# Kernel optimization log

Hardware: AMD Instinct MI355X
Metric: run time of the kernel (lower is better)

Reference implementation:

```python
import jax, jax.numpy as jnp
import numpy as np

LN_EPS = 1e-5

def _lstm_scan(xp, w_hh):
    # xp: [T, B, 4H] precomputed input projections (+bias); w_hh: [4H, H]
    H = w_hh.shape[1]
    B = xp.shape[1]
    def step(carry, x_t):
        h, c = carry
        gates = x_t + h @ w_hh.T
        i, f, g, o = jnp.split(gates, 4, axis=-1)  # torch gate order i,f,g,o
        i = jax.nn.sigmoid(i); f = jax.nn.sigmoid(f)
        g = jnp.tanh(g); o = jax.nn.sigmoid(o)
        c = f * c + i * g
        h = o * jnp.tanh(c)
        return (h, c), h
    init = (jnp.zeros((B, H), xp.dtype), jnp.zeros((B, H), xp.dtype))
    _, hs = jax.lax.scan(step, init, xp)
    return hs  # [T, B, H]

def setup_inputs() -> dict:
    key = jax.random.key(0)
    ks = jax.random.split(key, 16)
    B, T, V, E, K = 64, 512, 21128, 256, 9
    H4 = 4 * E
    s = 0.08  # small init scale for numerical stability
    return {
        'word_ids': jax.random.randint(ks[0], (B, T), 0, V, dtype=jnp.int32),
        'label_ids': jax.random.randint(ks[1], (B, T), 0, K, dtype=jnp.int32),
        'embed_table': jax.random.normal(ks[2], (V, E), jnp.float32) * s,
        'w_ih_f': jax.random.normal(ks[3], (H4, E), jnp.float32) * s,
        'w_hh_f': jax.random.normal(ks[4], (H4, E), jnp.float32) * s,
        'b_f': jnp.zeros((H4,), jnp.float32),
        'w_ih_b': jax.random.normal(ks[5], (H4, E), jnp.float32) * s,
        'w_hh_b': jax.random.normal(ks[6], (H4, E), jnp.float32) * s,
        'b_b': jnp.zeros((H4,), jnp.float32),
        'ln_gamma': jnp.ones((2 * E,), jnp.float32),
        'ln_beta': jnp.zeros((2 * E,), jnp.float32),
        'cls_w': jax.random.normal(ks[7], (K, 2 * E), jnp.float32) * s,
        'cls_b': jnp.zeros((K,), jnp.float32),
        'crf_start': jax.random.normal(ks[8], (K,), jnp.float32) * 0.1,
        'crf_end': jax.random.normal(ks[9], (K,), jnp.float32) * 0.1,
        'crf_trans': jax.random.normal(ks[10], (K, K), jnp.float32) * 0.1,
    }

def reference(word_ids, label_ids, embed_table, w_ih_f, w_hh_f, b_f,
              w_ih_b, w_hh_b, b_b, ln_gamma, ln_beta, cls_w, cls_b,
              crf_start, crf_end, crf_trans):
    # Embedding (dropout is identity at eval)
    emb = embed_table[word_ids]                      # [B, T, E]

    # BiLSTM: precompute input projections once, scan over time
    xf = (emb @ w_ih_f.T + b_f).transpose(1, 0, 2)   # [T, B, 4H]
    hf = _lstm_scan(xf, w_hh_f)                      # [T, B, H]
    xb = (emb[:, ::-1] @ w_ih_b.T + b_b).transpose(1, 0, 2)
    hb = _lstm_scan(xb, w_hh_b)[::-1]                # reverse back to forward time
    seq = jnp.concatenate([hf, hb], axis=-1).transpose(1, 0, 2)  # [B, T, 2H]

    # LayerNorm over last dim
    mu = seq.mean(-1, keepdims=True)
    var = ((seq - mu) ** 2).mean(-1, keepdims=True)
    seq = (seq - mu) * jax.lax.rsqrt(var + LN_EPS) * ln_gamma + ln_beta

    logits = seq @ cls_w.T + cls_b                   # [B, T, K] = CRF emissions

    # --- CRF log-likelihood (no mask: all positions valid) ---
    tags = label_ids
    # numerator: score of gold path
    em_score = jnp.take_along_axis(logits, tags[..., None], axis=-1)[..., 0]  # [B, T]
    trans_score = crf_trans[tags[:, :-1], tags[:, 1:]].sum(axis=1)            # [B]
    numerator = (crf_start[tags[:, 0]] + em_score.sum(axis=1)
                 + trans_score + crf_end[tags[:, -1]])                        # [B]

    # denominator: forward algorithm (logsumexp DP over time)
    alpha0 = crf_start[None, :] + logits[:, 0]       # [B, K]
    em_rest = logits[:, 1:].transpose(1, 0, 2)       # [T-1, B, K]
    def step(alpha, em_t):
        # alpha: [B, K] (prev tag), crf_trans: [K, K], em_t: [B, K] (next tag)
        new = jax.scipy.special.logsumexp(
            alpha[:, :, None] + crf_trans[None, :, :] + em_t[:, None, :], axis=1)
        return new, None
    alpha, _ = jax.lax.scan(step, alpha0, em_rest)
    logZ = jax.scipy.special.logsumexp(alpha + crf_end[None, :], axis=1)      # [B]

    llh = (numerator - logZ).sum()   # torchcrf default reduction='sum'
    loss = -llh
    preds = jnp.argmax(logits, axis=-1)
    return (loss, preds)
```

## Files before the change

kernel.cpp:

```cpp
#include <hip/hip_runtime.h>
#include <cstdint>
#include <cmath>

typedef __attribute__((ext_vector_type(8))) short short8;
typedef __attribute__((ext_vector_type(4))) float floatx4;

__device__ __forceinline__ unsigned pk_bf16(float x, float y) {
    unsigned ux = __float_as_uint(x); ux = ux + 0x7fffu + ((ux >> 16) & 1u);
    unsigned uy = __float_as_uint(y); uy = uy + 0x7fffu + ((uy >> 16) & 1u);
    return (ux >> 16) | (uy & 0xffff0000u);
}
__device__ __forceinline__ unsigned short bf16r(float x) {
    unsigned ux = __float_as_uint(x);
    return (unsigned short)((ux + 0x7fffu + ((ux >> 16) & 1u)) >> 16);
}
__device__ __forceinline__ float bf16d(unsigned short v) {
    return __uint_as_float((unsigned)v << 16);
}

__device__ __forceinline__ float fsigmoid(float x) {
    return __builtin_amdgcn_rcpf(1.f + __expf(-x));
}
__device__ __forceinline__ float ftanh(float x) {
    return 1.f - 2.f * __builtin_amdgcn_rcpf(__expf(2.f * x) + 1.f);
}

__device__ __forceinline__ void bar_lds() {
    __builtin_amdgcn_sched_barrier(0);
    asm volatile("s_waitcnt lgkmcnt(0)" ::: "memory");
    __builtin_amdgcn_s_barrier();
    __builtin_amdgcn_sched_barrier(0);
}

__global__ __launch_bounds__(256) void proj_kernel(
    const int* __restrict__ word_ids, const float* __restrict__ embed,
    const float* __restrict__ w_ih_f, const float* __restrict__ b_f,
    const float* __restrict__ w_ih_b, const float* __restrict__ b_b,
    unsigned short* __restrict__ XF, unsigned short* __restrict__ XB,
    int t0, int lgL)
{
    __shared__ unsigned short As[64][264];
    __shared__ unsigned short Bs[64][264];
    __shared__ int idx[64];

    const int tid = threadIdx.x;
    const int nt  = blockIdx.x;
    const int dir = blockIdx.y;
    const int Lm1 = (1 << lgL) - 1;
    const float* __restrict__ W    = dir ? w_ih_b : w_ih_f;
    const float* __restrict__ bias = dir ? b_b : b_f;
    unsigned short* __restrict__ Xout = dir ? XB : XF;

    if (tid < 64) {
        int n  = nt * 64 + tid;
        int b  = n >> lgL;
        int tl = n & Lm1;
        int tg = dir ? (511 - (t0 + tl)) : (t0 + tl);
        idx[tid] = word_ids[b * 512 + tg];
    }
    __syncthreads();

    #pragma unroll
    for (int i = 0; i < 16; ++i) {
        int flat = i * 256 + tid;
        int r  = flat >> 6;
        int kq = flat & 63;
        floatx4 a = *(const floatx4*)&embed[(size_t)idx[r] * 256 + kq * 4];
        *(uint2*)&As[r][kq * 4] = make_uint2(pk_bf16(a.x, a.y), pk_bf16(a.z, a.w));
    }
    __syncthreads();

    const int w    = tid >> 6;
    const int lane = tid & 63;
    const int q    = lane >> 4;
    const int lr   = lane & 15;

    short8 af[8];
    #pragma unroll
    for (int ks = 0; ks < 8; ++ks)
        af[ks] = *(const short8*)&As[w * 16 + lr][ks * 32 + q * 8];

    int bb[4], tt4[4];
    #pragma unroll
    for (int reg = 0; reg < 4; ++reg) {
        int n  = nt * 64 + w * 16 + q * 4 + reg;
        bb[reg]  = n >> lgL;
        tt4[reg] = n & Lm1;
    }

    for (int jt = 0; jt < 16; ++jt) {
        __syncthreads();
        #pragma unroll
        for (int i = 0; i < 16; ++i) {
            int flat = i * 256 + tid;
            int r  = flat >> 6;
            int kq = flat & 63;
            floatx4 wv = *(const floatx4*)&W[(size_t)(jt * 64 + r) * 256 + kq * 4];
            *(uint2*)&Bs[r][kq * 4] = make_uint2(pk_bf16(wv.x, wv.y), pk_bf16(wv.z, wv.w));
        }
        __syncthreads();

        #pragma unroll
        for (int jt4 = 0; jt4 < 4; ++jt4) {
            floatx4 c = {0.f, 0.f, 0.f, 0.f};
            #pragma unroll
            for (int ks = 0; ks < 8; ++ks) {
                short8 bf = *(const short8*)&Bs[jt4 * 16 + lr][ks * 32 + q * 8];
                c = __builtin_amdgcn_mfma_f32_16x16x32_bf16(af[ks], bf, c, 0, 0, 0);
            }
            int j = jt * 64 + jt4 * 16 + lr;
            float bj = bias[j];
            #pragma unroll
            for (int reg = 0; reg < 4; ++reg)
                Xout[((size_t)tt4[reg] * 64 + bb[reg]) * 1024 + j] = bf16r(c[reg] + bj);
        }
    }
}

#define LSTM_STEP(T, P, XG)                                                   \
    {                                                                         \
        floatx4 c[4][2];                                                      \
        _Pragma("unroll")                                                     \
        for (int gt = 0; gt < 4; ++gt) { c[gt][0] = zero; c[gt][1] = zero; }  \
        _Pragma("unroll")                                                     \
        for (int ks = 0; ks < 8; ++ks) {                                      \
            short8 af = *(const short8*)&Ah[P][lr & 1][ks * 32 + q * 8];      \
            _Pragma("unroll")                                                 \
            for (int nt = 0; nt < 8; ++nt) {                                  \
                const int gt = nt >> 1, ut = nt & 1;                          \
                short8 bf = (nt < 6) ? wreg[nt][ks]                           \
                                     : Wlds[((w * 2 + (nt - 6)) * 8 + ks) * 64 + lane]; \
                c[gt][ut] = __builtin_amdgcn_mfma_f32_16x16x32_bf16(          \
                    af, bf, c[gt][ut], 0, 0, 0);                              \
            }                                                                 \
        }                                                                     \
        float gsum[4];                                                        \
        _Pragma("unroll")                                                     \
        for (int gt = 0; gt < 4; ++gt) {                                      \
            float a0 = bsel ? c[gt][0][1] : c[gt][0][0];                      \
            float a1 = bsel ? c[gt][1][1] : c[gt][1][0];                      \
            gsum[gt] = (utsel ? a1 : a0) + XG[gt];                            \
        }                                                                     \
        {   \
            int tn = ((T) + 2 < t1) ? ((T) + 2 - t0) : 0;                     \
            const unsigned short* Xc =                                        \
                &X[((size_t)tn * 64 + B0 + b_own) * 1024 + u_own];            \
            _Pragma("unroll")                                                 \
            for (int gg = 0; gg < 4; ++gg) XG[gg] = bf16d(Xc[gg * 256]);      \
        }                                                                     \
        {                                                                     \
            float ig = fsigmoid(gsum[0]);                                     \
            float fg = fsigmoid(gsum[1]);                                     \
            float gc = ftanh(gsum[2]);                                        \
            float og = fsigmoid(gsum[3]);                                     \
            cst = fg * cst + ig * gc;                                         \
            float h = og * ftanh(cst);                                        \
            hlast = h;                                                        \
            Ah[(P) ^ 1][b_own][u_own] = bf16r(h);                             \
            int tt = dir ? (511 - (T)) : (T);                                 \
            Hout[((size_t)tt * 64 + B0 + b_own) * 256 + u_own] = h;           \
        }                                                                     \
        bar_lds();                                                            \
    }

__global__ __launch_bounds__(512, 1)
__attribute__((amdgpu_num_vgpr(256)))
void lstm_scan(
    const unsigned short* __restrict__ XF, const unsigned short* __restrict__ XB,
    const float* __restrict__ w_hh_f, const float* __restrict__ w_hh_b,
    float* __restrict__ hf, float* __restrict__ hb,
    float* __restrict__ state_c, float* __restrict__ state_h, int t0, int t1)
{
    __shared__ unsigned short Ah[2][2][264];
    __shared__ short8 Wlds[8 * 2 * 8 * 64];

    const int blk = blockIdx.x;
    const int dir = blk >> 5;
    const int grp = blk & 31;
    const int B0  = grp * 2;
    const unsigned short* __restrict__ X = dir ? XB : XF;
    const float* __restrict__ Whh = dir ? w_hh_b : w_hh_f;
    float* __restrict__ Hout      = dir ? hb : hf;

    const int tid  = threadIdx.x;
    const int w    = tid >> 6;
    const int lane = tid & 63;
    const int q    = lane >> 4;
    const int lr   = lane & 15;

    short8 wreg[6][8];
    #pragma unroll
    for (int nt = 0; nt < 8; ++nt) {
        const int gt = nt >> 1, ut = nt & 1;
        const float* wrow = &Whh[(size_t)(gt * 256 + w * 32 + ut * 16 + lr) * 256];
        #pragma unroll
        for (int ks = 0; ks < 8; ++ks) {
            floatx4 a = *(const floatx4*)&wrow[ks * 32 + q * 8];
            floatx4 b = *(const floatx4*)&wrow[ks * 32 + q * 8 + 4];
            union { uint4 u4; short8 s; } cv;
            cv.u4 = make_uint4(pk_bf16(a.x, a.y), pk_bf16(a.z, a.w),
                               pk_bf16(b.x, b.y), pk_bf16(b.z, b.w));
            if (nt < 6) wreg[nt][ks] = cv.s;
            else        Wlds[((w * 2 + (nt - 6)) * 8 + ks) * 64 + lane] = cv.s;
        }
    }

    const int b_own = lane >> 5;
    const int u_own = w * 32 + (lane & 31);
    const int sgi   = (dir * 64 + B0 + b_own) * 256 + u_own;

    float cst = 0.f, hlast = 0.f;
    if (t0 != 0) { cst = state_c[sgi]; hlast = state_h[sgi]; }
    Ah[t0 & 1][b_own][u_own] = bf16r(hlast);

    float xga[4], xgb[4];
    {
        const unsigned short* Xc0 = &X[((size_t)(B0 + b_own)) * 1024 + u_own];
        #pragma unroll
        for (int gg = 0; gg < 4; ++gg) xga[gg] = bf16d(Xc0[gg * 256]);
        const unsigned short* Xc1 = &X[((size_t)(64 + B0 + b_own)) * 1024 + u_own];
        #pragma unroll
        for (int gg = 0; gg < 4; ++gg) xgb[gg] = bf16d(Xc1[gg * 256]);
    }
    bar_lds();

    const floatx4 zero = {0.f, 0.f, 0.f, 0.f};
    const bool utsel = ((lane >> 4) & 1) != 0;
    const bool bsel  = (lane >> 5) != 0;

    for (int t = t0; t < t1; t += 2) {
        LSTM_STEP(t,     0, xga)
        LSTM_STEP(t + 1, 1, xgb)
    }

    state_c[sgi] = cst;
    state_h[sgi] = hlast;
}

__global__ __launch_bounds__(256) void ln_cls_kernel(
    const float* __restrict__ hf, const float* __restrict__ hb,
    const float* __restrict__ gamma, const float* __restrict__ beta,
    const float* __restrict__ cls_w, const float* __restrict__ cls_b,
    float* __restrict__ logits, float* __restrict__ dout)
{
    const int lane = threadIdx.x & 63;
    const int wid  = threadIdx.x >> 6;
    const int pos  = blockIdx.x * 4 + wid;
    const int b = pos >> 9;
    const int t = pos & 511;

    float4 v0 = *(const float4*)&hf[((size_t)t * 64 + b) * 256 + lane * 4];
    float4 v1 = *(const float4*)&hb[((size_t)t * 64 + b) * 256 + lane * 4];
    float x[8] = {v0.x, v0.y, v0.z, v0.w, v1.x, v1.y, v1.z, v1.w};

    float s = 0.f;
    #pragma unroll
    for (int i = 0; i < 8; ++i) s += x[i];
    #pragma unroll
    for (int off = 32; off > 0; off >>= 1) s += __shfl_xor(s, off, 64);
    float mu = s * (1.f / 512.f);

    float d[8];
    float sq = 0.f;
    #pragma unroll
    for (int i = 0; i < 8; ++i) { d[i] = x[i] - mu; sq += d[i] * d[i]; }
    #pragma unroll
    for (int off = 32; off > 0; off >>= 1) sq += __shfl_xor(sq, off, 64);
    float rs = 1.f / sqrtf(sq * (1.f / 512.f) + 1e-5f);

    float4 g0  = *(const float4*)&gamma[lane * 4];
    float4 g1  = *(const float4*)&gamma[256 + lane * 4];
    float4 be0 = *(const float4*)&beta[lane * 4];
    float4 be1 = *(const float4*)&beta[256 + lane * 4];
    float y[8];
    y[0] = d[0] * rs * g0.x + be0.x; y[1] = d[1] * rs * g0.y + be0.y;
    y[2] = d[2] * rs * g0.z + be0.z; y[3] = d[3] * rs * g0.w + be0.w;
    y[4] = d[4] * rs * g1.x + be1.x; y[5] = d[5] * rs * g1.y + be1.y;
    y[6] = d[6] * rs * g1.z + be1.z; y[7] = d[7] * rs * g1.w + be1.w;

    float lgt[9];
    #pragma unroll
    for (int c = 0; c < 9; ++c) {
        float4 w0 = *(const float4*)&cls_w[c * 512 + lane * 4];
        float4 w1 = *(const float4*)&cls_w[c * 512 + 256 + lane * 4];
        float p = y[0] * w0.x + y[1] * w0.y + y[2] * w0.z + y[3] * w0.w
                + y[4] * w1.x + y[5] * w1.y + y[6] * w1.z + y[7] * w1.w;
        #pragma unroll
        for (int off = 32; off > 0; off >>= 1) p += __shfl_xor(p, off, 64);
        lgt[c] = p + cls_b[c];
    }
    if (lane == 0) {
        int bestc = 0;
        float bestv = lgt[0];
        #pragma unroll
        for (int c = 1; c < 9; ++c)
            if (lgt[c] > bestv) { bestv = lgt[c]; bestc = c; }
        dout[1 + pos] = (float)bestc;
        #pragma unroll
        for (int c = 0; c < 9; ++c) logits[(size_t)pos * 9 + c] = lgt[c];
    }
}

__global__ __launch_bounds__(64) void crf_kernel(
    const float* __restrict__ logits, const int* __restrict__ label_ids,
    const float* __restrict__ crf_start, const float* __restrict__ crf_end,
    const float* __restrict__ crf_trans, float* __restrict__ llh)
{
    __shared__ float Ts[9][12];
    const int b = blockIdx.x;
    const int lane = threadIdx.x;
    if (lane < 81) Ts[lane / 9][lane % 9] = crf_trans[lane];
    __syncthreads();

    const float* __restrict__ em  = &logits[(size_t)b * 512 * 9];
    const int* __restrict__ tags  = &label_ids[b * 512];

    float part = 0.f;
    for (int t = lane; t < 512; t += 64) {
        int tg = tags[t];
        part += em[t * 9 + tg];
        if (t < 511) part += Ts[tg][tags[t + 1]];
    }
    #pragma unroll
    for (int off = 32; off > 0; off >>= 1) part += __shfl_xor(part, off, 64);
    float numer = part + crf_start[tags[0]] + crf_end[tags[511]];

    const int j = (lane < 9) ? lane : 0;
    float alpha = crf_start[j] + em[j];
    for (int t = 1; t < 512; ++t) {
        float av[9];
        float m = -1e30f;
        #pragma unroll
        for (int i = 0; i < 9; ++i) {
            float ai = __shfl(alpha, i, 64);
            av[i] = ai + Ts[i][j];
            m = fmaxf(m, av[i]);
        }
        float ssum = 0.f;
        #pragma unroll
        for (int i = 0; i < 9; ++i) ssum += expf(av[i] - m);
        alpha = m + logf(ssum) + em[t * 9 + j];
    }
    float v = (lane < 9) ? (alpha + crf_end[j]) : -1e30f;
    float mm = v;
    #pragma unroll
    for (int off = 32; off > 0; off >>= 1) mm = fmaxf(mm, __shfl_xor(mm, off, 64));
    float es = (lane < 9) ? expf(v - mm) : 0.f;
    #pragma unroll
    for (int off = 32; off > 0; off >>= 1) es += __shfl_xor(es, off, 64);
    if (lane == 0) llh[b] = numer - (mm + logf(es));
}

__global__ __launch_bounds__(64) void final_reduce(
    const float* __restrict__ llh, float* __restrict__ dout)
{
    float v = llh[threadIdx.x];
    #pragma unroll
    for (int off = 32; off > 0; off >>= 1) v += __shfl_xor(v, off, 64);
    if (threadIdx.x == 0) dout[0] = -v;
}

extern "C" void kernel_launch(void* const* d_in, const int* in_sizes, int n_in,
                              void* d_out, int out_size, void* d_ws, size_t ws_size,
                              hipStream_t stream)
{
    const int*   word_ids  = (const int*)d_in[0];
    const int*   label_ids = (const int*)d_in[1];
    const float* embed     = (const float*)d_in[2];
    const float* w_ih_f    = (const float*)d_in[3];
    const float* w_hh_f    = (const float*)d_in[4];
    const float* b_f       = (const float*)d_in[5];
    const float* w_ih_b    = (const float*)d_in[6];
    const float* w_hh_b    = (const float*)d_in[7];
    const float* b_b       = (const float*)d_in[8];
    const float* ln_gamma  = (const float*)d_in[9];
    const float* ln_beta   = (const float*)d_in[10];
    const float* cls_w     = (const float*)d_in[11];
    const float* cls_b     = (const float*)d_in[12];
    const float* crf_start = (const float*)d_in[13];
    const float* crf_end   = (const float*)d_in[14];
    const float* crf_trans = (const float*)d_in[15];

    char* w = (char*)d_ws;
    auto alloc = [&](size_t bytes) -> char* {
        char* p = w; w += (bytes + 255) & ~(size_t)255; return p;
    };
    float* hf      = (float*)alloc((size_t)8388608 * 4);
    float* hb      = (float*)alloc((size_t)8388608 * 4);
    float* logits  = (float*)alloc((size_t)294912 * 4);
    float* state_c = (float*)alloc((size_t)32768 * 4);
    float* state_h = (float*)alloc((size_t)32768 * 4);
    float* llh     = (float*)alloc((size_t)64 * 4);
    size_t fixed   = (size_t)(w - (char*)d_ws);

    int L = 512;
    while (L > 32 && fixed + (size_t)L * 262144 > ws_size) L >>= 1;
    unsigned short* XF = (unsigned short*)alloc((size_t)L * 65536 * 2);
    unsigned short* XB = (unsigned short*)alloc((size_t)L * 65536 * 2);
    int lgL = 31 - __builtin_clz((unsigned)L);

    for (int t0 = 0; t0 < 512; t0 += L) {
        proj_kernel<<<dim3(L, 2), 256, 0, stream>>>(
            word_ids, embed, w_ih_f, b_f, w_ih_b, b_b, XF, XB, t0, lgL);
        lstm_scan<<<64, 512, 0, stream>>>(
            XF, XB, w_hh_f, w_hh_b, hf, hb, state_c, state_h, t0, t0 + L);
    }
    ln_cls_kernel<<<8192, 256, 0, stream>>>(
        hf, hb, ln_gamma, ln_beta, cls_w, cls_b, logits, (float*)d_out);
    crf_kernel<<<64, 64, 0, stream>>>(
        logits, label_ids, crf_start, crf_end, crf_trans, llh);
    final_reduce<<<1, 64, 0, stream>>>(llh, (float*)d_out);
}
```

Measured before the change: 1.394 ms.

## Overlap next-chunk input projection with LSTM scan in one fused launch

The time axis is split into four fixed chunks of 128 steps, with double-buffered projection outputs. Each launch runs the recurrent scan for chunk c in 64 blocks while extra blocks compute the bf16 input projections for chunk c+1, so projection work hides behind the latency-bound serial scan instead of running between scans. It also fixes the chunk size regardless of workspace and raises shared memory per block to about 133 KB to fit two GEMM units. The risk is that projection blocks compete with scan blocks for memory bandwidth and CU resources, and the chunked scan adds launch and state save/restore overhead.

```diff
diff --git a/kernel.cpp b/kernel.cpp
--- a/kernel.cpp
+++ b/kernel.cpp
@@ -165,76 +165,166 @@
 
 __global__ __launch_bounds__(512, 1)
 __attribute__((amdgpu_num_vgpr(256)))
-void lstm_scan(
-    const unsigned short* __restrict__ XF, const unsigned short* __restrict__ XB,
+void fused_scan_proj(
+    const unsigned short* __restrict__ XFc, const unsigned short* __restrict__ XBc,
     const float* __restrict__ w_hh_f, const float* __restrict__ w_hh_b,
     float* __restrict__ hf, float* __restrict__ hb,
-    float* __restrict__ state_c, float* __restrict__ state_h, int t0, int t1)
+    float* __restrict__ state_c, float* __restrict__ state_h, int t0, int t1,
+    const int* __restrict__ word_ids, const float* __restrict__ embed,
+    const float* __restrict__ w_ih_f, const float* __restrict__ b_f,
+    const float* __restrict__ w_ih_b, const float* __restrict__ b_b,
+    unsigned short* __restrict__ XFn, unsigned short* __restrict__ XBn,
+    int pt0, int lgL)
 {
-    __shared__ unsigned short Ah[2][2][264];
-    __shared__ short8 Wlds[8 * 2 * 8 * 64];
-
-    const int blk = blockIdx.x;
-    const int dir = blk >> 5;
-    const int grp = blk & 31;
-    const int B0  = grp * 2;
-    const unsigned short* __restrict__ X = dir ? XB : XF;
-    const float* __restrict__ Whh = dir ? w_hh_b : w_hh_f;
-    float* __restrict__ Hout      = dir ? hb : hf;
-
-    const int tid  = threadIdx.x;
-    const int w    = tid >> 6;
-    const int lane = tid & 63;
-    const int q    = lane >> 4;
-    const int lr   = lane & 15;
-
-    short8 wreg[6][8];
-    #pragma unroll
-    for (int nt = 0; nt < 8; ++nt) {
-        const int gt = nt >> 1, ut = nt & 1;
-        const float* wrow = &Whh[(size_t)(gt * 256 + w * 32 + ut * 16 + lr) * 256];
-        #pragma unroll
-        for (int ks = 0; ks < 8; ++ks) {
-            floatx4 a = *(const floatx4*)&wrow[ks * 32 + q * 8];
-            floatx4 b = *(const floatx4*)&wrow[ks * 32 + q * 8 + 4];
-            union { uint4 u4; short8 s; } cv;
-            cv.u4 = make_uint4(pk_bf16(a.x, a.y), pk_bf16(a.z, a.w),
-                               pk_bf16(b.x, b.y), pk_bf16(b.z, b.w));
-            if (nt < 6) wreg[nt][ks] = cv.s;
-            else        Wlds[((w * 2 + (nt - 6)) * 8 + ks) * 64 + lane] = cv.s;
-        }
-    }
-
-    const int b_own = lane >> 5;
-    const int u_own = w * 32 + (lane & 31);
-    const int sgi   = (dir * 64 + B0 + b_own) * 256 + u_own;
-
-    float cst = 0.f, hlast = 0.f;
-    if (t0 != 0) { cst = state_c[sgi]; hlast = state_h[sgi]; }
-    Ah[t0 & 1][b_own][u_own] = bf16r(hlast);
-
-    float xga[4], xgb[4];
-    {
-        const unsigned short* Xc0 = &X[((size_t)(B0 + b_own)) * 1024 + u_own];
-        #pragma unroll
-        for (int gg = 0; gg < 4; ++gg) xga[gg] = bf16d(Xc0[gg * 256]);
-        const unsigned short* Xc1 = &X[((size_t)(64 + B0 + b_own)) * 1024 + u_own];
-        #pragma unroll
-        for (int gg = 0; gg < 4; ++gg) xgb[gg] = bf16d(Xc1[gg * 256]);
-    }
-    bar_lds();
-
-    const floatx4 zero = {0.f, 0.f, 0.f, 0.f};
-    const bool utsel = ((lane >> 4) & 1) != 0;
-    const bool bsel  = (lane >> 5) != 0;
-
-    for (int t = t0; t < t1; t += 2) {
-        LSTM_STEP(t,     0, xga)
-        LSTM_STEP(t + 1, 1, xgb)
-    }
-
-    state_c[sgi] = cst;
-    state_h[sgi] = hlast;
+    __shared__ __align__(16) char smem[135936];
+
+    if (blockIdx.x < 64) {
+        unsigned short (*Ah)[2][264] = (unsigned short (*)[2][264])smem;
+        short8* Wlds = (short8*)(smem + 2112);
+
+        const int blk = blockIdx.x;
+        const int dir = blk >> 5;
+        const int grp = blk & 31;
+        const int B0  = grp * 2;
+        const unsigned short* __restrict__ X = dir ? XBc : XFc;
+        const float* __restrict__ Whh = dir ? w_hh_b : w_hh_f;
+        float* __restrict__ Hout      = dir ? hb : hf;
+
+        const int tid  = threadIdx.x;
+        const int w    = tid >> 6;
+        const int lane = tid & 63;
+        const int q    = lane >> 4;
+        const int lr   = lane & 15;
+
+        short8 wreg[6][8];
+        #pragma unroll
+        for (int nt = 0; nt < 8; ++nt) {
+            const int gt = nt >> 1, ut = nt & 1;
+            const float* wrow = &Whh[(size_t)(gt * 256 + w * 32 + ut * 16 + lr) * 256];
+            #pragma unroll
+            for (int ks = 0; ks < 8; ++ks) {
+                floatx4 a = *(const floatx4*)&wrow[ks * 32 + q * 8];
+                floatx4 b = *(const floatx4*)&wrow[ks * 32 + q * 8 + 4];
+                union { uint4 u4; short8 s; } cv;
+                cv.u4 = make_uint4(pk_bf16(a.x, a.y), pk_bf16(a.z, a.w),
+                                   pk_bf16(b.x, b.y), pk_bf16(b.z, b.w));
+                if (nt < 6) wreg[nt][ks] = cv.s;
+                else        Wlds[((w * 2 + (nt - 6)) * 8 + ks) * 64 + lane] = cv.s;
+            }
+        }
+
+        const int b_own = lane >> 5;
+        const int u_own = w * 32 + (lane & 31);
+        const int sgi   = (dir * 64 + B0 + b_own) * 256 + u_own;
+
+        float cst = 0.f, hlast = 0.f;
+        if (t0 != 0) { cst = state_c[sgi]; hlast = state_h[sgi]; }
+        Ah[t0 & 1][b_own][u_own] = bf16r(hlast);
+
+        float xga[4], xgb[4];
+        {
+            const unsigned short* Xc0 = &X[((size_t)(B0 + b_own)) * 1024 + u_own];
+            #pragma unroll
+            for (int gg = 0; gg < 4; ++gg) xga[gg] = bf16d(Xc0[gg * 256]);
+            const unsigned short* Xc1 = &X[((size_t)(64 + B0 + b_own)) * 1024 + u_own];
+            #pragma unroll
+            for (int gg = 0; gg < 4; ++gg) xgb[gg] = bf16d(Xc1[gg * 256]);
+        }
+        bar_lds();
+
+        const floatx4 zero = {0.f, 0.f, 0.f, 0.f};
+        const bool utsel = ((lane >> 4) & 1) != 0;
+        const bool bsel  = (lane >> 5) != 0;
+
+        for (int t = t0; t < t1; t += 2) {
+            LSTM_STEP(t,     0, xga)
+            LSTM_STEP(t + 1, 1, xgb)
+        }
+
+        state_c[sgi] = cst;
+        state_h[sgi] = hlast;
+    } else {
+        const int unit = threadIdx.x >> 8;
+        const int tid  = threadIdx.x & 255;
+        const int uidx = (blockIdx.x - 64) * 2 + unit;
+        const int dir  = uidx & 1;
+        const int nt   = uidx >> 1;
+        const int Lm1  = (1 << lgL) - 1;
+
+        char* base = smem + unit * 67968;
+        unsigned short (*As)[264] = (unsigned short (*)[264])base;
+        unsigned short (*Bs)[264] = (unsigned short (*)[264])(base + 33792);
+        int* idx = (int*)(base + 67584);
+
+        const float* __restrict__ W    = dir ? w_ih_b : w_ih_f;
+        const float* __restrict__ bias = dir ? b_b : b_f;
+        unsigned short* __restrict__ Xout = dir ? XBn : XFn;
+
+        if (tid < 64) {
+            int n  = nt * 64 + tid;
+            int b  = n >> lgL;
+            int tl = n & Lm1;
+            int tg = dir ? (511 - (pt0 + tl)) : (pt0 + tl);
+            idx[tid] = word_ids[b * 512 + tg];
+        }
+        __syncthreads();
+
+        #pragma unroll
+        for (int i = 0; i < 16; ++i) {
+            int flat = i * 256 + tid;
+            int r  = flat >> 6;
+            int kq = flat & 63;
+            floatx4 a = *(const floatx4*)&embed[(size_t)idx[r] * 256 + kq * 4];
+            *(uint2*)&As[r][kq * 4] = make_uint2(pk_bf16(a.x, a.y), pk_bf16(a.z, a.w));
+        }
+        __syncthreads();
+
+        const int w    = tid >> 6;
+        const int lane = tid & 63;
+        const int q    = lane >> 4;
+        const int lr   = lane & 15;
+
+        short8 af[8];
+        #pragma unroll
+        for (int ks = 0; ks < 8; ++ks)
+            af[ks] = *(const short8*)&As[w * 16 + lr][ks * 32 + q * 8];
+
+        int bb[4], tt4[4];
+        #pragma unroll
+        for (int reg = 0; reg < 4; ++reg) {
+            int n  = nt * 64 + w * 16 + q * 4 + reg;
+            bb[reg]  = n >> lgL;
+            tt4[reg] = n & Lm1;
+        }
+
+        for (int jt = 0; jt < 16; ++jt) {
+            __syncthreads();
+            #pragma unroll
+            for (int i = 0; i < 16; ++i) {
+                int flat = i * 256 + tid;
+                int r  = flat >> 6;
+                int kq = flat & 63;
+                floatx4 wv = *(const floatx4*)&W[(size_t)(jt * 64 + r) * 256 + kq * 4];
+                *(uint2*)&Bs[r][kq * 4] = make_uint2(pk_bf16(wv.x, wv.y), pk_bf16(wv.z, wv.w));
+            }
+            __syncthreads();
+
+            #pragma unroll
+            for (int jt4 = 0; jt4 < 4; ++jt4) {
+                floatx4 c = {0.f, 0.f, 0.f, 0.f};
+                #pragma unroll
+                for (int ks = 0; ks < 8; ++ks) {
+                    short8 bf = *(const short8*)&Bs[jt4 * 16 + lr][ks * 32 + q * 8];
+                    c = __builtin_amdgcn_mfma_f32_16x16x32_bf16(af[ks], bf, c, 0, 0, 0);
+                }
+                int j = jt * 64 + jt4 * 16 + lr;
+                float bj = bias[j];
+                #pragma unroll
+                for (int reg = 0; reg < 4; ++reg)
+                    Xout[((size_t)tt4[reg] * 64 + bb[reg]) * 1024 + j] = bf16r(c[reg] + bj);
+            }
+        }
+    }
 }
 
 __global__ __launch_bounds__(256) void ln_cls_kernel(
@@ -391,20 +481,29 @@
     float* state_c = (float*)alloc((size_t)32768 * 4);
     float* state_h = (float*)alloc((size_t)32768 * 4);
     float* llh     = (float*)alloc((size_t)64 * 4);
-    size_t fixed   = (size_t)(w - (char*)d_ws);
-
-    int L = 512;
-    while (L > 32 && fixed + (size_t)L * 262144 > ws_size) L >>= 1;
-    unsigned short* XF = (unsigned short*)alloc((size_t)L * 65536 * 2);
-    unsigned short* XB = (unsigned short*)alloc((size_t)L * 65536 * 2);
-    int lgL = 31 - __builtin_clz((unsigned)L);
-
-    for (int t0 = 0; t0 < 512; t0 += L) {
-        proj_kernel<<<dim3(L, 2), 256, 0, stream>>>(
-            word_ids, embed, w_ih_f, b_f, w_ih_b, b_b, XF, XB, t0, lgL);
-        lstm_scan<<<64, 512, 0, stream>>>(
-            XF, XB, w_hh_f, w_hh_b, hf, hb, state_c, state_h, t0, t0 + L);
-    }
+
+    const int L   = 128;
+    const int lgL = 7;
+    const size_t chunkElems = (size_t)L * 65536;
+    unsigned short* XF = (unsigned short*)alloc(2 * chunkElems * 2);
+    unsigned short* XB = (unsigned short*)alloc(2 * chunkElems * 2);
+
+    proj_kernel<<<dim3(L, 2), 256, 0, stream>>>(
+        word_ids, embed, w_ih_f, b_f, w_ih_b, b_b, XF, XB, 0, lgL);
+
+    for (int c = 0; c < 4; ++c) {
+        const unsigned short* XFc = XF + (size_t)(c & 1) * chunkElems;
+        const unsigned short* XBc = XB + (size_t)(c & 1) * chunkElems;
+        unsigned short* XFn = XF + (size_t)((c + 1) & 1) * chunkElems;
+        unsigned short* XBn = XB + (size_t)((c + 1) & 1) * chunkElems;
+        int grid = (c < 3) ? 64 + L : 64;
+        fused_scan_proj<<<grid, 512, 0, stream>>>(
+            XFc, XBc, w_hh_f, w_hh_b, hf, hb, state_c, state_h,
+            c * L, (c + 1) * L,
+            word_ids, embed, w_ih_f, b_f, w_ih_b, b_b, XFn, XBn,
+            (c + 1) * L, lgL);
+    }
+
     ln_cls_kernel<<<8192, 256, 0, stream>>>(
         hf, hb, ln_gamma, ln_beta, cls_w, cls_b, logits, (float*)d_out);
     crf_kernel<<<64, 64, 0, stream>>>(
```

After: 1.580 ms. 1.13x slower.

## Fuse input projection and LSTM scan into one persistent producer-consumer kernel

Applied to the files above, without the earlier changes.

Merges the projection GEMM and the recurrent LSTM scan into a single persistent launch. 64 blocks run the scan while 128 blocks compute input projections in 128-step chunks and signal readiness through atomic flags. The scan waits on each chunk's flag, so projection of later chunks overlaps the serial recurrence and the separate launches plus carried-state round trips go away. The design relies on all 192 blocks being co-resident to avoid deadlock, needs full-length X buffers, and drops the chunked fallback for small workspaces.

```diff
diff --git a/kernel.cpp b/kernel.cpp
--- a/kernel.cpp
+++ b/kernel.cpp
@@ -30,91 +30,6 @@
     asm volatile("s_waitcnt lgkmcnt(0)" ::: "memory");
     __builtin_amdgcn_s_barrier();
     __builtin_amdgcn_sched_barrier(0);
-}
-
-__global__ __launch_bounds__(256) void proj_kernel(
-    const int* __restrict__ word_ids, const float* __restrict__ embed,
-    const float* __restrict__ w_ih_f, const float* __restrict__ b_f,
-    const float* __restrict__ w_ih_b, const float* __restrict__ b_b,
-    unsigned short* __restrict__ XF, unsigned short* __restrict__ XB,
-    int t0, int lgL)
-{
-    __shared__ unsigned short As[64][264];
-    __shared__ unsigned short Bs[64][264];
-    __shared__ int idx[64];
-
-    const int tid = threadIdx.x;
-    const int nt  = blockIdx.x;
-    const int dir = blockIdx.y;
-    const int Lm1 = (1 << lgL) - 1;
-    const float* __restrict__ W    = dir ? w_ih_b : w_ih_f;
-    const float* __restrict__ bias = dir ? b_b : b_f;
-    unsigned short* __restrict__ Xout = dir ? XB : XF;
-
-    if (tid < 64) {
-        int n  = nt * 64 + tid;
-        int b  = n >> lgL;
-        int tl = n & Lm1;
-        int tg = dir ? (511 - (t0 + tl)) : (t0 + tl);
-        idx[tid] = word_ids[b * 512 + tg];
-    }
-    __syncthreads();
-
-    #pragma unroll
-    for (int i = 0; i < 16; ++i) {
-        int flat = i * 256 + tid;
-        int r  = flat >> 6;
-        int kq = flat & 63;
-        floatx4 a = *(const floatx4*)&embed[(size_t)idx[r] * 256 + kq * 4];
-        *(uint2*)&As[r][kq * 4] = make_uint2(pk_bf16(a.x, a.y), pk_bf16(a.z, a.w));
-    }
-    __syncthreads();
-
-    const int w    = tid >> 6;
-    const int lane = tid & 63;
-    const int q    = lane >> 4;
-    const int lr   = lane & 15;
-
-    short8 af[8];
-    #pragma unroll
-    for (int ks = 0; ks < 8; ++ks)
-        af[ks] = *(const short8*)&As[w * 16 + lr][ks * 32 + q * 8];
-
-    int bb[4], tt4[4];
-    #pragma unroll
-    for (int reg = 0; reg < 4; ++reg) {
-        int n  = nt * 64 + w * 16 + q * 4 + reg;
-        bb[reg]  = n >> lgL;
-        tt4[reg] = n & Lm1;
-    }
-
-    for (int jt = 0; jt < 16; ++jt) {
-        __syncthreads();
-        #pragma unroll
-        for (int i = 0; i < 16; ++i) {
-            int flat = i * 256 + tid;
-            int r  = flat >> 6;
-            int kq = flat & 63;
-            floatx4 wv = *(const floatx4*)&W[(size_t)(jt * 64 + r) * 256 + kq * 4];
-            *(uint2*)&Bs[r][kq * 4] = make_uint2(pk_bf16(wv.x, wv.y), pk_bf16(wv.z, wv.w));
-        }
-        __syncthreads();
-
-        #pragma unroll
-        for (int jt4 = 0; jt4 < 4; ++jt4) {
-            floatx4 c = {0.f, 0.f, 0.f, 0.f};
-            #pragma unroll
-            for (int ks = 0; ks < 8; ++ks) {
-                short8 bf = *(const short8*)&Bs[jt4 * 16 + lr][ks * 32 + q * 8];
-                c = __builtin_amdgcn_mfma_f32_16x16x32_bf16(af[ks], bf, c, 0, 0, 0);
-            }
-            int j = jt * 64 + jt4 * 16 + lr;
-            float bj = bias[j];
-            #pragma unroll
-            for (int reg = 0; reg < 4; ++reg)
-                Xout[((size_t)tt4[reg] * 64 + bb[reg]) * 1024 + j] = bf16r(c[reg] + bj);
-        }
-    }
 }
 
 #define LSTM_STEP(T, P, XG)                                                   \
@@ -141,8 +56,8 @@
             float a1 = bsel ? c[gt][1][1] : c[gt][1][0];                      \
             gsum[gt] = (utsel ? a1 : a0) + XG[gt];                            \
         }                                                                     \
-        {   \
-            int tn = ((T) + 2 < t1) ? ((T) + 2 - t0) : 0;                     \
+        {               \
+            int tn = ((T) + 2 < 512) ? ((T) + 2) : 0;                         \
             const unsigned short* Xc =                                        \
                 &X[((size_t)tn * 64 + B0 + b_own) * 1024 + u_own];            \
             _Pragma("unroll")                                                 \
@@ -165,76 +80,183 @@
 
 __global__ __launch_bounds__(512, 1)
 __attribute__((amdgpu_num_vgpr(256)))
-void lstm_scan(
-    const unsigned short* __restrict__ XF, const unsigned short* __restrict__ XB,
+void fused_persistent(
+    unsigned short* __restrict__ XF, unsigned short* __restrict__ XB,
     const float* __restrict__ w_hh_f, const float* __restrict__ w_hh_b,
     float* __restrict__ hf, float* __restrict__ hb,
-    float* __restrict__ state_c, float* __restrict__ state_h, int t0, int t1)
+    const int* __restrict__ word_ids, const float* __restrict__ embed,
+    const float* __restrict__ w_ih_f, const float* __restrict__ b_f,
+    const float* __restrict__ w_ih_b, const float* __restrict__ b_b,
+    int* __restrict__ flags)
 {
-    __shared__ unsigned short Ah[2][2][264];
-    __shared__ short8 Wlds[8 * 2 * 8 * 64];
-
-    const int blk = blockIdx.x;
-    const int dir = blk >> 5;
-    const int grp = blk & 31;
-    const int B0  = grp * 2;
-    const unsigned short* __restrict__ X = dir ? XB : XF;
-    const float* __restrict__ Whh = dir ? w_hh_b : w_hh_f;
-    float* __restrict__ Hout      = dir ? hb : hf;
-
-    const int tid  = threadIdx.x;
-    const int w    = tid >> 6;
-    const int lane = tid & 63;
-    const int q    = lane >> 4;
-    const int lr   = lane & 15;
-
-    short8 wreg[6][8];
-    #pragma unroll
-    for (int nt = 0; nt < 8; ++nt) {
-        const int gt = nt >> 1, ut = nt & 1;
-        const float* wrow = &Whh[(size_t)(gt * 256 + w * 32 + ut * 16 + lr) * 256];
-        #pragma unroll
-        for (int ks = 0; ks < 8; ++ks) {
-            floatx4 a = *(const floatx4*)&wrow[ks * 32 + q * 8];
-            floatx4 b = *(const floatx4*)&wrow[ks * 32 + q * 8 + 4];
-            union { uint4 u4; short8 s; } cv;
-            cv.u4 = make_uint4(pk_bf16(a.x, a.y), pk_bf16(a.z, a.w),
-                               pk_bf16(b.x, b.y), pk_bf16(b.z, b.w));
-            if (nt < 6) wreg[nt][ks] = cv.s;
-            else        Wlds[((w * 2 + (nt - 6)) * 8 + ks) * 64 + lane] = cv.s;
-        }
-    }
-
-    const int b_own = lane >> 5;
-    const int u_own = w * 32 + (lane & 31);
-    const int sgi   = (dir * 64 + B0 + b_own) * 256 + u_own;
-
-    float cst = 0.f, hlast = 0.f;
-    if (t0 != 0) { cst = state_c[sgi]; hlast = state_h[sgi]; }
-    Ah[t0 & 1][b_own][u_own] = bf16r(hlast);
-
-    float xga[4], xgb[4];
-    {
-        const unsigned short* Xc0 = &X[((size_t)(B0 + b_own)) * 1024 + u_own];
-        #pragma unroll
-        for (int gg = 0; gg < 4; ++gg) xga[gg] = bf16d(Xc0[gg * 256]);
-        const unsigned short* Xc1 = &X[((size_t)(64 + B0 + b_own)) * 1024 + u_own];
-        #pragma unroll
-        for (int gg = 0; gg < 4; ++gg) xgb[gg] = bf16d(Xc1[gg * 256]);
-    }
-    bar_lds();
-
-    const floatx4 zero = {0.f, 0.f, 0.f, 0.f};
-    const bool utsel = ((lane >> 4) & 1) != 0;
-    const bool bsel  = (lane >> 5) != 0;
-
-    for (int t = t0; t < t1; t += 2) {
-        LSTM_STEP(t,     0, xga)
-        LSTM_STEP(t + 1, 1, xgb)
-    }
-
-    state_c[sgi] = cst;
-    state_h[sgi] = hlast;
+    __shared__ __align__(16) char smem[135936];
+
+    if (blockIdx.x < 64) {
+        unsigned short (*Ah)[2][264] = (unsigned short (*)[2][264])smem;
+        short8* Wlds = (short8*)(smem + 2112);
+
+        const int blk = blockIdx.x;
+        const int dir = blk >> 5;
+        const int grp = blk & 31;
+        const int B0  = grp * 2;
+        const unsigned short* __restrict__ X = dir ? XB : XF;
+        const float* __restrict__ Whh = dir ? w_hh_b : w_hh_f;
+        float* __restrict__ Hout      = dir ? hb : hf;
+
+        const int tid  = threadIdx.x;
+        const int w    = tid >> 6;
+        const int lane = tid & 63;
+        const int q    = lane >> 4;
+        const int lr   = lane & 15;
+
+        short8 wreg[6][8];
+        #pragma unroll
+        for (int nt = 0; nt < 8; ++nt) {
+            const int gt = nt >> 1, ut = nt & 1;
+            const float* wrow = &Whh[(size_t)(gt * 256 + w * 32 + ut * 16 + lr) * 256];
+            #pragma unroll
+            for (int ks = 0; ks < 8; ++ks) {
+                floatx4 a = *(const floatx4*)&wrow[ks * 32 + q * 8];
+                floatx4 b = *(const floatx4*)&wrow[ks * 32 + q * 8 + 4];
+                union { uint4 u4; short8 s; } cv;
+                cv.u4 = make_uint4(pk_bf16(a.x, a.y), pk_bf16(a.z, a.w),
+                                   pk_bf16(b.x, b.y), pk_bf16(b.z, b.w));
+                if (nt < 6) wreg[nt][ks] = cv.s;
+                else        Wlds[((w * 2 + (nt - 6)) * 8 + ks) * 64 + lane] = cv.s;
+            }
+        }
+
+        if (tid == 0) {
+            while (__hip_atomic_load(&flags[0], __ATOMIC_ACQUIRE,
+                                     __HIP_MEMORY_SCOPE_AGENT) < 128)
+                __builtin_amdgcn_s_sleep(2);
+        }
+        __syncthreads();
+
+        const int b_own = lane >> 5;
+        const int u_own = w * 32 + (lane & 31);
+
+        float cst = 0.f, hlast = 0.f;
+        Ah[0][b_own][u_own] = 0;
+
+        float xga[4], xgb[4];
+        {
+            const unsigned short* Xc0 = &X[((size_t)(B0 + b_own)) * 1024 + u_own];
+            #pragma unroll
+            for (int gg = 0; gg < 4; ++gg) xga[gg] = bf16d(Xc0[gg * 256]);
+            const unsigned short* Xc1 = &X[((size_t)(64 + B0 + b_own)) * 1024 + u_own];
+            #pragma unroll
+            for (int gg = 0; gg < 4; ++gg) xgb[gg] = bf16d(Xc1[gg * 256]);
+        }
+        bar_lds();
+
+        const floatx4 zero = {0.f, 0.f, 0.f, 0.f};
+        const bool utsel = ((lane >> 4) & 1) != 0;
+        const bool bsel  = (lane >> 5) != 0;
+
+        for (int t = 0; t < 512; t += 2) {
+            if ((t & 127) == 126 && t + 2 < 512) {
+                if (tid == 0) {
+                    while (__hip_atomic_load(&flags[(t + 2) >> 7], __ATOMIC_ACQUIRE,
+                                             __HIP_MEMORY_SCOPE_AGENT) < 128)
+                        __builtin_amdgcn_s_sleep(2);
+                }
+                __syncthreads();
+            }
+            LSTM_STEP(t,     0, xga)
+            LSTM_STEP(t + 1, 1, xgb)
+        }
+    } else {
+        const int unit = threadIdx.x >> 8;
+        const int tid  = threadIdx.x & 255;
+        const int uidx = (blockIdx.x - 64) * 2 + unit;
+        const int dir  = uidx & 1;
+        const int nt   = uidx >> 1;
+
+        char* base = smem + unit * 67968;
+        unsigned short (*As)[264] = (unsigned short (*)[264])base;
+        unsigned short (*Bs)[264] = (unsigned short (*)[264])(base + 33792);
+        int* idx = (int*)(base + 67584);
+
+        const float* __restrict__ W    = dir ? w_ih_b : w_ih_f;
+        const float* __restrict__ bias = dir ? b_b : b_f;
+        unsigned short* __restrict__ Xout = dir ? XB : XF;
+
+        const int w    = tid >> 6;
+        const int lane = tid & 63;
+        const int q    = lane >> 4;
+        const int lr   = lane & 15;
+
+        int bb[4], tt4[4];
+        #pragma unroll
+        for (int reg = 0; reg < 4; ++reg) {
+            int n  = nt * 64 + w * 16 + q * 4 + reg;
+            bb[reg]  = n >> 7;
+            tt4[reg] = n & 127;
+        }
+
+        for (int pc = 0; pc < 4; ++pc) {
+            const int pt0 = pc * 128;
+
+            if (tid < 64) {
+                int n  = nt * 64 + tid;
+                int b  = n >> 7;
+                int tl = n & 127;
+                int tg = dir ? (511 - (pt0 + tl)) : (pt0 + tl);
+                idx[tid] = word_ids[b * 512 + tg];
+            }
+            __syncthreads();
+
+            #pragma unroll
+            for (int i = 0; i < 16; ++i) {
+                int flat = i * 256 + tid;
+                int r  = flat >> 6;
+                int kq = flat & 63;
+                floatx4 a = *(const floatx4*)&embed[(size_t)idx[r] * 256 + kq * 4];
+                *(uint2*)&As[r][kq * 4] = make_uint2(pk_bf16(a.x, a.y), pk_bf16(a.z, a.w));
+            }
+            __syncthreads();
+
+            short8 af[8];
+            #pragma unroll
+            for (int ks = 0; ks < 8; ++ks)
+                af[ks] = *(const short8*)&As[w * 16 + lr][ks * 32 + q * 8];
+
+            for (int jt = 0; jt < 16; ++jt) {
+                __syncthreads();
+                #pragma unroll
+                for (int i = 0; i < 16; ++i) {
+                    int flat = i * 256 + tid;
+                    int r  = flat >> 6;
+                    int kq = flat & 63;
+                    floatx4 wv = *(const floatx4*)&W[(size_t)(jt * 64 + r) * 256 + kq * 4];
+                    *(uint2*)&Bs[r][kq * 4] = make_uint2(pk_bf16(wv.x, wv.y), pk_bf16(wv.z, wv.w));
+                }
+                __syncthreads();
+
+                #pragma unroll
+                for (int jt4 = 0; jt4 < 4; ++jt4) {
+                    floatx4 c = {0.f, 0.f, 0.f, 0.f};
+                    #pragma unroll
+                    for (int ks = 0; ks < 8; ++ks) {
+                        short8 bf = *(const short8*)&Bs[jt4 * 16 + lr][ks * 32 + q * 8];
+                        c = __builtin_amdgcn_mfma_f32_16x16x32_bf16(af[ks], bf, c, 0, 0, 0);
+                    }
+                    int j = jt * 64 + jt4 * 16 + lr;
+                    float bj = bias[j];
+                    #pragma unroll
+                    for (int reg = 0; reg < 4; ++reg)
+                        Xout[((size_t)(pt0 + tt4[reg]) * 64 + bb[reg]) * 1024 + j] =
+                            bf16r(c[reg] + bj);
+                }
+            }
+
+            __syncthreads();
+            if (threadIdx.x == 0)
+                __hip_atomic_fetch_add(&flags[pc], 1, __ATOMIC_RELEASE,
+                                       __HIP_MEMORY_SCOPE_AGENT);
+        }
+    }
 }
 
 __global__ __launch_bounds__(256) void ln_cls_kernel(
@@ -388,23 +410,17 @@
     float* hf      = (float*)alloc((size_t)8388608 * 4);
     float* hb      = (float*)alloc((size_t)8388608 * 4);
     float* logits  = (float*)alloc((size_t)294912 * 4);
-    float* state_c = (float*)alloc((size_t)32768 * 4);
-    float* state_h = (float*)alloc((size_t)32768 * 4);
     float* llh     = (float*)alloc((size_t)64 * 4);
-    size_t fixed   = (size_t)(w - (char*)d_ws);
-
-    int L = 512;
-    while (L > 32 && fixed + (size_t)L * 262144 > ws_size) L >>= 1;
-    unsigned short* XF = (unsigned short*)alloc((size_t)L * 65536 * 2);
-    unsigned short* XB = (unsigned short*)alloc((size_t)L * 65536 * 2);
-    int lgL = 31 - __builtin_clz((unsigned)L);
-
-    for (int t0 = 0; t0 < 512; t0 += L) {
-        proj_kernel<<<dim3(L, 2), 256, 0, stream>>>(
-            word_ids, embed, w_ih_f, b_f, w_ih_b, b_b, XF, XB, t0, lgL);
-        lstm_scan<<<64, 512, 0, stream>>>(
-            XF, XB, w_hh_f, w_hh_b, hf, hb, state_c, state_h, t0, t0 + L);
-    }
+    int*   flags   = (int*)alloc(4 * sizeof(int));
+    unsigned short* XF = (unsigned short*)alloc((size_t)512 * 65536 * 2);
+    unsigned short* XB = (unsigned short*)alloc((size_t)512 * 65536 * 2);
+
+    hipMemsetAsync(flags, 0, 4 * sizeof(int), stream);
+
+    fused_persistent<<<192, 512, 0, stream>>>(
+        XF, XB, w_hh_f, w_hh_b, hf, hb,
+        word_ids, embed, w_ih_f, b_f, w_ih_b, b_b, flags);
+
     ln_cls_kernel<<<8192, 256, 0, stream>>>(
         hf, hb, ln_gamma, ln_beta, cls_w, cls_b, logits, (float*)d_out);
     crf_kernel<<<64, 64, 0, stream>>>(
```

New measurement: 3.981 ms. 2.86x slower.
